# Optimization experiments

Measured on AMD Instinct MI355X. Metric: run time of the kernel, lower is better.

Reference implementation:

```python
import jax, jax.numpy as jnp
import numpy as np

B, L, HID = 2, 2048, 2048
N_HEAD, HEAD_DIM, N_KV = 32, 64, 8
N_Q_PER_KV = N_HEAD // N_KV  # 4
SCALE = 0.125  # 1/sqrt(HEAD_DIM)
PAD_START = L - 256  # last 256 key positions are padding
NEG = -1e9


def setup_inputs() -> dict:
    key = jax.random.key(0)
    ks = jax.random.split(key, 8)
    query = jax.random.normal(ks[0], (B, L, HID), jnp.float32)
    kv = jax.random.normal(ks[1], (B, L, HID), jnp.float32)
    # additive causal mask (0 on/below diagonal, -1e9 above)
    i = jnp.arange(L)
    attn_mask = jnp.where(i[None, :] > i[:, None], NEG, 0.0).astype(jnp.float32)
    # key padding mask: True == padded position
    key_padding_mask = (i[None, :] >= PAD_START) & jnp.ones((B, 1), bool)
    s = 0.02
    Wq = jax.random.normal(ks[2], (HID, N_HEAD * HEAD_DIM), jnp.float32) * s
    bq = jnp.zeros((N_HEAD * HEAD_DIM,), jnp.float32)
    Wkv = jax.random.normal(ks[3], (HID, 2 * N_KV * HEAD_DIM), jnp.float32) * s
    bkv = jnp.zeros((2 * N_KV * HEAD_DIM,), jnp.float32)
    Wo = jax.random.normal(ks[4], (N_HEAD * HEAD_DIM, HID), jnp.float32) * s
    bo = jnp.zeros((HID,), jnp.float32)
    return {"query": query, "kv": kv, "Wq": Wq, "bq": bq, "Wkv": Wkv,
            "bkv": bkv, "Wo": Wo, "bo": bo, "attn_mask": attn_mask,
            "key_padding_mask": key_padding_mask}


def reference(query, kv, Wq, bq, Wkv, bkv, Wo, bo, attn_mask, key_padding_mask):
    b, l, _ = query.shape
    q = (query @ Wq + bq).reshape(b, l, N_HEAD, HEAD_DIM).transpose(0, 2, 1, 3)  # [B,H,L,D]
    kvp = kv @ Wkv + bkv                                   # [B,L,2*NKV*D]
    k, v = jnp.split(kvp, 2, axis=-1)
    k = k.reshape(b, l, N_KV, HEAD_DIM)
    v = v.reshape(b, l, N_KV, HEAD_DIM)
    # GQA: repeat_interleave KV heads to match Q heads
    k = jnp.repeat(k, N_Q_PER_KV, axis=2).transpose(0, 2, 1, 3)  # [B,H,L,D]
    v = jnp.repeat(v, N_Q_PER_KV, axis=2).transpose(0, 2, 1, 3)
    qk = jnp.einsum('bhqd,bhkd->bhqk', q, k) * SCALE
    qk = qk + attn_mask                                     # additive mask
    qk = jnp.where(key_padding_mask[:, None, None, :], NEG, qk)
    p = jax.nn.softmax(qk.astype(jnp.float32), axis=-1).astype(q.dtype)
    attn = jnp.einsum('bhqk,bhkd->bhqd', p, v)
    attn = attn.transpose(0, 2, 1, 3).reshape(b, l, N_HEAD * HEAD_DIM)
    out = attn @ Wo + bo
    return out
```

## Files before the change

### kernel.cpp

```cpp
#include <hip/hip_runtime.h>
#include <stdint.h>

#define L_SEQ 2048
#define HID 2048
#define PADK 1792
#define QSCALE 0.18033688011112042f

typedef unsigned short us_t;
typedef __attribute__((ext_vector_type(8))) short bf16x8;
typedef __attribute__((ext_vector_type(4))) float f32x4;

__device__ __forceinline__ float bf2f(us_t u) {
    union { unsigned int i; float f; } c; c.i = ((unsigned int)u) << 16; return c.f;
}
__device__ __forceinline__ us_t f2bf(float f) {
    union { float f; unsigned int i; } c; c.f = f;
    unsigned int i = c.i;
    return (us_t)((i + 0x7FFFu + ((i >> 16) & 1u)) >> 16);
}
__device__ __forceinline__ unsigned int pk_bf16(float a, float b) {
#if __has_builtin(__builtin_amdgcn_cvt_pk_bf16_f32)
    auto r = __builtin_amdgcn_cvt_pk_bf16_f32(a, b);
    unsigned int u; __builtin_memcpy(&u, &r, 4); return u;
#else
    return (unsigned int)f2bf(a) | ((unsigned int)f2bf(b) << 16);
#endif
}
__device__ __forceinline__ float fast_exp2(float x) {
#if __has_builtin(__builtin_amdgcn_exp2f)
    return __builtin_amdgcn_exp2f(x);
#else
    return exp2f(x);
#endif
}
__device__ __forceinline__ void gload_lds16(const us_t* g, us_t* l) {
    __builtin_amdgcn_global_load_lds((const __attribute__((address_space(1))) void*)g,
                                     (__attribute__((address_space(3))) void*)l, 16, 0, 0);
}
__device__ __forceinline__ int detect_bf16(const unsigned int* q) {
    __shared__ int sc[4];
    unsigned int v = q[threadIdx.x & 255];
    unsigned int e = (v >> 7) & 0xFFu;
    unsigned long long bb = __ballot(e >= 112u && e <= 133u);
    int cnt = __popcll(bb);
    if ((threadIdx.x & 63) == 0) sc[threadIdx.x >> 6] = cnt;
    __syncthreads();
    return (sc[0] + sc[1] + sc[2] + sc[3]) > 128;
}
__device__ __forceinline__ int detect_bf16_512(const unsigned int* q) {
    __shared__ int sc[8];
    unsigned int v = q[threadIdx.x & 255];
    unsigned int e = (v >> 7) & 0xFFu;
    unsigned long long bb = __ballot(e >= 112u && e <= 133u);
    int cnt = __popcll(bb);
    if ((threadIdx.x & 63) == 0) sc[threadIdx.x >> 6] = cnt;
    __syncthreads();
    int s = 0;
    #pragma unroll
    for (int i = 0; i < 8; ++i) s += sc[i];
    return s > 256;
}

__global__ __launch_bounds__(256) void prep(const unsigned int* __restrict__ qdet,
                                            const void* __restrict__ query,
                                            const void* __restrict__ kvsrc,
                                            const void* __restrict__ Wq,
                                            const void* __restrict__ Wkv,
                                            const void* __restrict__ Wo,
                                            us_t* __restrict__ Aq, us_t* __restrict__ Akv,
                                            us_t* __restrict__ Wqt, us_t* __restrict__ Wkvt,
                                            us_t* __restrict__ Wot) {
    __shared__ us_t tile[64][65];
    const int bf = detect_bf16(qdet);
    int id = blockIdx.x;
    if (id < 8192) {
        const void* s = (id < 4096) ? query : kvsrc;
        us_t* d       = (id < 4096) ? Aq : Akv;
        int cid = (id & 4095) * 256 + threadIdx.x;
        if (bf) {
            ((bf16x8*)d)[cid] = ((const bf16x8*)s)[cid];
        } else {
            const float* sp = (const float*)s + (size_t)cid * 8;
            f32x4 a = *(const f32x4*)sp, b2 = *(const f32x4*)(sp + 4);
            union { bf16x8 v; unsigned int dw[4]; } o;
            o.dw[0] = pk_bf16(a[0], a[1]);   o.dw[1] = pk_bf16(a[2], a[3]);
            o.dw[2] = pk_bf16(b2[0], b2[1]); o.dw[3] = pk_bf16(b2[2], b2[3]);
            ((bf16x8*)d)[cid] = o.v;
        }
        return;
    }
    id -= 8192;
    const void* s; us_t* d; int R, C, bx, by;
    if (id < 1024)      { s = Wq;  d = Wqt;  R = 2048; C = 2048; bx = id & 31; by = id >> 5; }
    else if (id < 1536) { id -= 1024; s = Wkv; d = Wkvt; R = 2048; C = 1024; bx = id & 15; by = id >> 4; }
    else                { id -= 1536; s = Wo;  d = Wot;  R = 2048; C = 2048; bx = id & 31; by = id >> 5; }
    const int c0 = bx * 64, r0 = by * 64;
    #pragma unroll
    for (int i = 0; i < 16; ++i) {
        int idx = threadIdx.x + i * 256;
        int r = idx >> 6, c = idx & 63;
        tile[r][c] = bf ? ((const us_t*)s)[(size_t)(r0 + r) * C + c0 + c]
                        : f2bf(((const float*)s)[(size_t)(r0 + r) * C + c0 + c]);
    }
    __syncthreads();
    #pragma unroll
    for (int i = 0; i < 16; ++i) {
        int idx = threadIdx.x + i * 256;
        int c = idx >> 6, r = idx & 63;
        d[(size_t)(c0 + c) * R + r0 + r] = tile[r][c];
    }
}

template<int MQ, int NQ, typename STG, typename TAIL>
__device__ __forceinline__ void phase8(const us_t* Ab, const us_t* Bb,
                                       int wm, int wn, int l15, int cs0, int cs1,
                                       f32x4 (&acc)[8][4], STG&& stg, TAIL&& tail) {
    bf16x8 af[4][2], bv[2][2];
    #pragma unroll
    for (int mt = 0; mt < 4; ++mt) {
        const us_t* p = &Ab[(wm * 128 + MQ * 64 + mt * 16 + l15) * 64];
        af[mt][0] = *(const bf16x8*)&p[cs0 * 8];
        af[mt][1] = *(const bf16x8*)&p[cs1 * 8];
    }
    #pragma unroll
    for (int nt = 0; nt < 2; ++nt) {
        const us_t* p = &Bb[(wn * 64 + NQ * 32 + nt * 16 + l15) * 64];
        bv[nt][0] = *(const bf16x8*)&p[cs0 * 8];
        bv[nt][1] = *(const bf16x8*)&p[cs1 * 8];
    }
    stg();
    __builtin_amdgcn_s_barrier();
    asm volatile("s_waitcnt lgkmcnt(0)" ::: "memory");
    __builtin_amdgcn_sched_barrier(0);
    __builtin_amdgcn_s_setprio(1);
    #pragma unroll
    for (int ki = 0; ki < 2; ++ki)
        #pragma unroll
        for (int mt = 0; mt < 4; ++mt)
            #pragma unroll
            for (int nt = 0; nt < 2; ++nt)
                acc[MQ * 4 + mt][NQ * 2 + nt] = __builtin_amdgcn_mfma_f32_16x16x32_bf16(
                    af[mt][ki], bv[nt][ki], acc[MQ * 4 + mt][NQ * 2 + nt], 0, 0, 0);
    __builtin_amdgcn_s_setprio(0);
    tail();
    __builtin_amdgcn_s_barrier();
}

__global__ __launch_bounds__(512, 2) void qkv_gemm(const unsigned int* __restrict__ qdet,
                                                   const us_t* __restrict__ Aq,
                                                   const us_t* __restrict__ Akv,
                                                   const us_t* __restrict__ Wqt,
                                                   const us_t* __restrict__ Wkvt,
                                                   const void* __restrict__ bq,
                                                   const void* __restrict__ bkv,
                                                   us_t* __restrict__ Qm,
                                                   us_t* __restrict__ Km,
                                                   us_t* __restrict__ Vg) {
    __shared__ us_t sh[65536];
    us_t* As0 = sh;
    us_t* As1 = sh + 16384;
    us_t* Bs0 = sh + 32768;
    us_t* Bs1 = sh + 49152;

    const int bf = detect_bf16_512(qdet);
    const int t = threadIdx.x;
    const int w = t >> 6, lane = t & 63, l15 = lane & 15, quad = lane >> 4;
    const int wm = w >> 2, wn = w & 3;
    const int cs0 = quad ^ (l15 & 7);
    const int cs1 = (4 + quad) ^ (l15 & 7);

    int id = blockIdx.x;
    const us_t* Ag; const us_t* Bg; int bm, bn; bool isQ;
    if (id < 128) { isQ = true;  Ag = Aq;  Bg = Wqt;  bm = (id >> 3) * 256; bn = (id & 7) * 256; }
    else { id -= 128; isQ = false; Ag = Akv; Bg = Wkvt; bm = (id >> 2) * 256; bn = (id & 3) * 256; }

    size_t aoff[2][2], boff[2][2]; int adst[2][2], bdst[2][2];
    #pragma unroll
    for (int u = 0; u < 2; ++u)
        #pragma unroll
        for (int j = 0; j < 2; ++j) {
            int row0 = j * 128 + u * 64 + w * 8;
            int row  = row0 + (lane >> 3);
            int col  = ((lane & 7) ^ (row & 7)) * 8;
            aoff[u][j] = (size_t)(bm + row) * 2048 + col;
            adst[u][j] = row0 * 64;
            int ci   = w * 2 + j;
            int rb0  = (ci >> 2) * 64 + u * 32 + (ci & 3) * 8;
            int rowb = rb0 + (lane >> 3);
            int colb = ((lane & 7) ^ (rowb & 7)) * 8;
            boff[u][j] = (size_t)(bn + rowb) * 2048 + colb;
            bdst[u][j] = rb0 * 64;
        }

#define STAGE_A(U, KT, DST) do { \
        gload_lds16(Ag + aoff[U][0] + (size_t)(KT) * 64, (DST) + adst[U][0]); \
        gload_lds16(Ag + aoff[U][1] + (size_t)(KT) * 64, (DST) + adst[U][1]); } while (0)
#define STAGE_B(U, KT, DST) do { \
        gload_lds16(Bg + boff[U][0] + (size_t)(KT) * 64, (DST) + bdst[U][0]); \
        gload_lds16(Bg + boff[U][1] + (size_t)(KT) * 64, (DST) + bdst[U][1]); } while (0)

    f32x4 acc[8][4];
    #pragma unroll
    for (int i = 0; i < 8; ++i)
        #pragma unroll
        for (int j = 0; j < 4; ++j) acc[i][j] = (f32x4){0.f, 0.f, 0.f, 0.f};

    STAGE_A(0, 0, As0); STAGE_B(0, 0, Bs0);
    STAGE_A(1, 0, As0); STAGE_B(1, 0, Bs0);
    STAGE_A(0, 1, As1); STAGE_B(0, 1, Bs1);
    asm volatile("s_waitcnt vmcnt(4)" ::: "memory");
    __builtin_amdgcn_s_barrier();

    auto notail = [] {};
    #pragma unroll 1
    for (int it = 0; it < 16; ++it) {
        const bool more = (it < 15);
        const int k1 = 2 * it + 1, k2 = 2 * it + 2, k3 = 2 * it + 3;
        phase8<0, 0>(As0, Bs0, wm, wn, l15, cs0, cs1, acc,
                     [&] { STAGE_A(1, k1, As1); }, notail);
        phase8<0, 1>(As0, Bs0, wm, wn, l15, cs0, cs1, acc,
                     [&] { STAGE_B(1, k1, Bs1); }, notail);
        phase8<1, 0>(As0, Bs0, wm, wn, l15, cs0, cs1, acc,
                     [&] { if (more) STAGE_A(0, k2, As0); }, notail);
        phase8<1, 1>(As0, Bs0, wm, wn, l15, cs0, cs1, acc,
                     [&] { if (more) STAGE_B(0, k2, Bs0); },
                     [&] { if (more) asm volatile("s_waitcnt vmcnt(4)" ::: "memory");
                           else      asm volatile("s_waitcnt vmcnt(0)" ::: "memory"); });
        phase8<0, 0>(As1, Bs1, wm, wn, l15, cs0, cs1, acc,
                     [&] { if (more) STAGE_A(1, k2, As0); }, notail);
        phase8<0, 1>(As1, Bs1, wm, wn, l15, cs0, cs1, acc,
                     [&] { if (more) STAGE_B(1, k2, Bs0); }, notail);
        phase8<1, 0>(As1, Bs1, wm, wn, l15, cs0, cs1, acc,
                     [&] { if (more) STAGE_A(0, k3, As1); }, notail);
        phase8<1, 1>(As1, Bs1, wm, wn, l15, cs0, cs1, acc,
                     [&] { if (more) STAGE_B(0, k3, Bs1); },
                     [&] { if (more) asm volatile("s_waitcnt vmcnt(4)" ::: "memory"); });
    }
#undef STAGE_A
#undef STAGE_B

    if (isQ) {
        #pragma unroll
        for (int an = 0; an < 4; ++an) {
            int col = bn + wn * 64 + an * 16 + l15;
            float bvv = bf ? bf2f(((const us_t*)bq)[col]) : ((const float*)bq)[col];
            #pragma unroll
            for (int am = 0; am < 8; ++am)
                #pragma unroll
                for (int r = 0; r < 4; ++r) {
                    int row = bm + wm * 128 + am * 16 + quad * 4 + r;
                    Qm[(size_t)row * 2048 + col] = f2bf((acc[am][an][r] + bvv) * QSCALE);
                }
        }
    } else if (bn < 512) {
        #pragma unroll
        for (int an = 0; an < 4; ++an) {
            int col = bn + wn * 64 + an * 16 + l15;
            float bvv = bf ? bf2f(((const us_t*)bkv)[col]) : ((const float*)bkv)[col];
            #pragma unroll
            for (int am = 0; am < 8; ++am)
                #pragma unroll
                for (int r = 0; r < 4; ++r) {
                    int row = bm + wm * 128 + am * 16 + quad * 4 + r;
                    Km[(size_t)row * 512 + col] = f2bf(acc[am][an][r] + bvv);
                }
        }
    } else {
        const int b2 = bm >> 11, tok0 = bm & 2047;
        #pragma unroll
        for (int half = 0; half < 2; ++half) {
            __syncthreads();
            if ((wn >> 1) == half) {
                #pragma unroll
                for (int an = 0; an < 4; ++an) {
                    int col = bn + wn * 64 + an * 16 + l15;
                    float bvv = bf ? bf2f(((const us_t*)bkv)[col]) : ((const float*)bkv)[col];
                    int cl = (wn & 1) * 64 + an * 16 + l15;
                    #pragma unroll
                    for (int am = 0; am < 8; ++am)
                        #pragma unroll
                        for (int r = 0; r < 4; ++r) {
                            int tok = wm * 128 + am * 16 + quad * 4 + r;
                            sh[cl * 258 + tok] = f2bf(acc[am][an][r] + bvv);
                        }
                }
            }
            __syncthreads();
            size_t vrow0 = (size_t)(b2 * 512 + (bn - 512) + half * 128);
            #pragma unroll
            for (int jj = 0; jj < 8; ++jj) {
                int idx = t + jj * 512;
                int c2 = idx >> 5, ch = idx & 31;
                bf16x8 vv = *(const bf16x8*)&sh[c2 * 258 + ch * 8];
                *(bf16x8*)(Vg + (vrow0 + c2) * (size_t)2048 + tok0 + ch * 8) = vv;
            }
        }
    }
}

__device__ __forceinline__ void gemm_core(const us_t* __restrict__ A,
                                          const us_t* __restrict__ Bt,
                                          int K, int bm, int bn, int t,
                                          us_t (&As)[2][8192], us_t (&Bs)[2][8192],
                                          f32x4 (&acc)[4][4]) {
    const int w = t >> 6, lane = t & 63, l15 = lane & 15, quad = lane >> 4;
    const int wm = (w & 1) * 64, wn = (w >> 1) * 64;
    int rA[4], cA[4];
    #pragma unroll
    for (int i = 0; i < 4; ++i) {
        int p = (w * 4 + i) * 64 + lane;
        int row = p >> 3, cs = p & 7;
        rA[i] = row; cA[i] = (cs ^ (row & 7)) * 8;
    }
    #pragma unroll
    for (int i = 0; i < 4; ++i) {
        gload_lds16(A  + (size_t)(bm + rA[i]) * K + cA[i], &As[0][(w * 4 + i) * 512]);
        gload_lds16(Bt + (size_t)(bn + rA[i]) * K + cA[i], &Bs[0][(w * 4 + i) * 512]);
    }
    int pb = 0;
    for (int k0 = 0; k0 < K; k0 += 64) {
        __syncthreads();
        if (k0 + 64 < K) {
            #pragma unroll
            for (int i = 0; i < 4; ++i) {
                gload_lds16(A  + (size_t)(bm + rA[i]) * K + k0 + 64 + cA[i], &As[pb ^ 1][(w * 4 + i) * 512]);
                gload_lds16(Bt + (size_t)(bn + rA[i]) * K + k0 + 64 + cA[i], &Bs[pb ^ 1][(w * 4 + i) * 512]);
            }
        }
        #pragma unroll
        for (int ki = 0; ki < 2; ++ki) {
            bf16x8 af[4], bfr[4];
            #pragma unroll
            for (int mt = 0; mt < 4; ++mt) {
                int row = wm + mt * 16 + l15;
                int cs  = (ki * 4 + quad) ^ (row & 7);
                af[mt] = *(const bf16x8*)&As[pb][row * 64 + cs * 8];
            }
            #pragma unroll
            for (int nt = 0; nt < 4; ++nt) {
                int row = wn + nt * 16 + l15;
                int cs  = (ki * 4 + quad) ^ (row & 7);
                bfr[nt] = *(const bf16x8*)&Bs[pb][row * 64 + cs * 8];
            }
            #pragma unroll
            for (int mt = 0; mt < 4; ++mt)
                #pragma unroll
                for (int nt = 0; nt < 4; ++nt)
                    acc[mt][nt] = __builtin_amdgcn_mfma_f32_16x16x32_bf16(af[mt], bfr[nt], acc[mt][nt], 0, 0, 0);
        }
        pb ^= 1;
    }
}

__global__ __launch_bounds__(256, 2) void o_gemm(const unsigned int* __restrict__ qdet,
                                                 const us_t* __restrict__ Ao,
                                                 const us_t* __restrict__ Wot,
                                                 const void* __restrict__ bo,
                                                 void* __restrict__ Out) {
    __shared__ us_t As[2][8192], Bs[2][8192];
    const int bf = detect_bf16(qdet);
    const int t = threadIdx.x;
    const int w = t >> 6, lane = t & 63, l15 = lane & 15, quad = lane >> 4;
    const int wm = (w & 1) * 64, wn = (w >> 1) * 64;
    const int bm = blockIdx.y * 128, bn = blockIdx.x * 128;
    f32x4 acc[4][4];
    #pragma unroll
    for (int i = 0; i < 4; ++i)
        #pragma unroll
        for (int j = 0; j < 4; ++j) acc[i][j] = (f32x4){0.f, 0.f, 0.f, 0.f};
    gemm_core(Ao, Wot, 2048, bm, bn, t, As, Bs, acc);
    #pragma unroll
    for (int nt = 0; nt < 4; ++nt) {
        int col = bn + wn + nt * 16 + l15;
        float bvv = bf ? bf2f(((const us_t*)bo)[col]) : ((const float*)bo)[col];
        #pragma unroll
        for (int mt = 0; mt < 4; ++mt)
            #pragma unroll
            for (int r = 0; r < 4; ++r) {
                int row = bm + wm + mt * 16 + quad * 4 + r;
                float v = acc[mt][nt][r] + bvv;
                if (bf) ((us_t*)Out)[(size_t)row * 2048 + col] = f2bf(v);
                else    ((float*)Out)[(size_t)row * 2048 + col] = v;
            }
    }
}

__device__ __forceinline__ void qk_exp(const bf16x8 kb[2][4], const bf16x8 qf[2][2],
                                       int q0, int k0, int l15, int quad,
                                       bf16x8 pa[2][2]) {
    f32x4 sa[2][4];
    #pragma unroll
    for (int mt = 0; mt < 2; ++mt)
        #pragma unroll
        for (int nt = 0; nt < 4; ++nt) sa[mt][nt] = (f32x4){0.f, 0.f, 0.f, 0.f};
    #pragma unroll
    for (int ki = 0; ki < 2; ++ki)
        #pragma unroll
        for (int mt = 0; mt < 2; ++mt)
            #pragma unroll
            for (int nt = 0; nt < 4; ++nt)
                sa[mt][nt] = __builtin_amdgcn_mfma_f32_16x16x32_bf16(kb[ki][nt], qf[mt][ki], sa[mt][nt], 0, 0, 0);
    const bool nm = (k0 + 63 > q0);
    #pragma unroll
    for (int mt = 0; mt < 2; ++mt) {
        const int qrow = q0 + mt * 16 + l15;
        union { bf16x8 v; unsigned int dw[4]; } u;
        #pragma unroll
        for (int k2 = 0; k2 < 2; ++k2) {
            #pragma unroll
            for (int hf = 0; hf < 2; ++hf) {
                const int nt = k2 * 2 + hf;
                const int keyb = k0 + k2 * 32 + hf * 4 + quad * 8;
                float e[4];
                #pragma unroll
                for (int r = 0; r < 4; ++r) {
                    float s = sa[mt][nt][r];
                    if (nm && (keyb + r > qrow)) s = -1e30f;
                    e[r] = fast_exp2(s);
                }
                u.dw[hf * 2]     = pk_bf16(e[0], e[1]);
                u.dw[hf * 2 + 1] = pk_bf16(e[2], e[3]);
            }
            pa[mt][k2] = u.v;
        }
    }
}

__global__ __launch_bounds__(256, 2) void attn_mfma(const us_t* __restrict__ Q,
                                                    const us_t* __restrict__ Km,
                                                    const us_t* __restrict__ Vg,
                                                    us_t* __restrict__ Am) {
    __shared__ us_t Ks[2][4096];
    __shared__ us_t Vt[2][4096];

    const int bid = blockIdx.x;
    const int pr  = bid & 31;
    const int kvh = (bid >> 5) & 7;
    const int b   = bid >> 8;
    const int t = threadIdx.x, w = t >> 6, lane = t & 63, l15 = lane & 15, quad = lane >> 4;
    const int h = kvh * 4 + w;
    const int q0h = 2016 - 32 * pr, q0l = 32 * pr;
    const int kend0 = min(q0h + 32, PADK), kend1 = min(q0l + 32, PADK);

    bf16x8 ones;
    #pragma unroll
    for (int j = 0; j < 8; ++j) ones[j] = (short)0x3F80;

    const us_t* Kbase = Km + (size_t)(b * L_SEQ) * 512 + kvh * 64;
    const us_t* Vbase = Vg + (size_t)(b * 512 + kvh * 64) * L_SEQ;

    size_t ksrc[2], vsrc[2];
    #pragma unroll
    for (int i = 0; i < 2; ++i) {
        int idx = (w * 2 + i) * 64 + lane;
        int p = idx >> 3, cs = idx & 7, c = cs ^ (p & 7);
        int gk = (p & 0x23) | ((p & 0x0C) << 1) | ((p & 0x10) >> 2);
        ksrc[i] = (size_t)gk * 512 + c * 8;
        vsrc[i] = (size_t)p * 2048 + c * 8;
    }

    bf16x8 qfh[2][2], qfl[2][2];
    #pragma unroll
    for (int mt = 0; mt < 2; ++mt)
        #pragma unroll
        for (int ki = 0; ki < 2; ++ki) {
            qfh[mt][ki] = *(const bf16x8*)(Q + (size_t)(b * L_SEQ + q0h + mt * 16 + l15) * HID
                                             + h * 64 + ki * 32 + quad * 8);
            qfl[mt][ki] = *(const bf16x8*)(Q + (size_t)(b * L_SEQ + q0l + mt * 16 + l15) * HID
                                             + h * 64 + ki * 32 + quad * 8);
        }

    f32x4 oah[2][4], oal[2][4], lah[2], lal[2];
    #pragma unroll
    for (int mt = 0; mt < 2; ++mt) {
        lah[mt] = (f32x4){0.f, 0.f, 0.f, 0.f};
        lal[mt] = (f32x4){0.f, 0.f, 0.f, 0.f};
        #pragma unroll
        for (int dn = 0; dn < 4; ++dn) {
            oah[mt][dn] = (f32x4){0.f, 0.f, 0.f, 0.f};
            oal[mt][dn] = (f32x4){0.f, 0.f, 0.f, 0.f};
        }
    }

    #pragma unroll
    for (int i = 0; i < 2; ++i) {
        gload_lds16(Kbase + ksrc[i], &Ks[0][(w * 2 + i) * 512]);
        gload_lds16(Vbase + vsrc[i], &Vt[0][(w * 2 + i) * 512]);
    }

    int pb = 0;
    for (int k0 = 0; k0 < kend0; k0 += 64) {
        __syncthreads();
        if (k0 + 64 < kend0) {
            #pragma unroll
            for (int i = 0; i < 2; ++i) {
                gload_lds16(Kbase + (size_t)(k0 + 64) * 512 + ksrc[i], &Ks[pb ^ 1][(w * 2 + i) * 512]);
                gload_lds16(Vbase + (k0 + 64) + vsrc[i],               &Vt[pb ^ 1][(w * 2 + i) * 512]);
            }
        }
        const bool dolight = (k0 < kend1);

        bf16x8 kb[2][4];
        #pragma unroll
        for (int ki = 0; ki < 2; ++ki)
            #pragma unroll
            for (int nt = 0; nt < 4; ++nt) {
                int row = nt * 16 + l15;
                int cs  = (ki * 4 + quad) ^ (row & 7);
                kb[ki][nt] = *(const bf16x8*)&Ks[pb][row * 64 + cs * 8];
            }

        bf16x8 pah[2][2], pal[2][2];
        qk_exp(kb, qfh, q0h, k0, l15, quad, pah);
        if (dolight) qk_exp(kb, qfl, q0l, k0, l15, quad, pal);

        bf16x8 vb[2][4];
        #pragma unroll
        for (int k2 = 0; k2 < 2; ++k2)
            #pragma unroll
            for (int dn = 0; dn < 4; ++dn) {
                int d  = dn * 16 + l15;
                int cs = (k2 * 4 + quad) ^ (d & 7);
                vb[k2][dn] = *(const bf16x8*)&Vt[pb][d * 64 + cs * 8];
            }

        #pragma unroll
        for (int k2 = 0; k2 < 2; ++k2)
            #pragma unroll
            for (int mt = 0; mt < 2; ++mt) {
                lah[mt] = __builtin_amdgcn_mfma_f32_16x16x32_bf16(pah[mt][k2], ones, lah[mt], 0, 0, 0);
                #pragma unroll
                for (int dn = 0; dn < 4; ++dn)
                    oah[mt][dn] = __builtin_amdgcn_mfma_f32_16x16x32_bf16(pah[mt][k2], vb[k2][dn], oah[mt][dn], 0, 0, 0);
            }
        if (dolight) {
            #pragma unroll
            for (int k2 = 0; k2 < 2; ++k2)
                #pragma unroll
                for (int mt = 0; mt < 2; ++mt) {
                    lal[mt] = __builtin_amdgcn_mfma_f32_16x16x32_bf16(pal[mt][k2], ones, lal[mt], 0, 0, 0);
                    #pragma unroll
                    for (int dn = 0; dn < 4; ++dn)
                        oal[mt][dn] = __builtin_amdgcn_mfma_f32_16x16x32_bf16(pal[mt][k2], vb[k2][dn], oal[mt][dn], 0, 0, 0);
                }
        }
        pb ^= 1;
    }

    #pragma unroll
    for (int mt = 0; mt < 2; ++mt)
        #pragma unroll
        for (int r = 0; r < 4; ++r) {
            float invh = 1.0f / lah[mt][r];
            float invl = 1.0f / lal[mt][r];
            int rowh = q0h + mt * 16 + quad * 4 + r;
            int rowl = q0l + mt * 16 + quad * 4 + r;
            #pragma unroll
            for (int dn = 0; dn < 4; ++dn) {
                Am[(size_t)(b * L_SEQ + rowh) * HID + h * 64 + dn * 16 + l15] =
                    f2bf(oah[mt][dn][r] * invh);
                Am[(size_t)(b * L_SEQ + rowl) * HID + h * 64 + dn * 16 + l15] =
                    f2bf(oal[mt][dn][r] * invl);
            }
        }
}

extern "C" void kernel_launch(void* const* d_in, const int* in_sizes, int n_in,
                              void* d_out, int out_size, void* d_ws, size_t ws_size,
                              hipStream_t stream) {
    const void* query = d_in[0];
    const void* kv    = d_in[1];
    const void* Wq    = d_in[2];
    const void* bq    = d_in[3];
    const void* Wkv   = d_in[4];
    const void* bkv   = d_in[5];
    const void* Wo    = d_in[6];
    const void* bo    = d_in[7];
    const unsigned int* qdet = (const unsigned int*)query;

    char* p = (char*)d_ws;
    us_t* Qm   = (us_t*)p;                p += (size_t)4096 * 2048 * 2;
    us_t* Km   = (us_t*)p;                p += (size_t)4096 * 512 * 2;
    us_t* Vg   = (us_t*)p;                p += (size_t)1024 * 2048 * 2;
    us_t* AqAm = (us_t*)p;                p += (size_t)4096 * 2048 * 2;
    us_t* Akv  = (us_t*)p;                p += (size_t)4096 * 2048 * 2;
    us_t* Wqt  = (us_t*)p;                p += (size_t)2048 * 2048 * 2;
    us_t* Wkvt = (us_t*)p;                p += (size_t)1024 * 2048 * 2;
    us_t* Wot  = (us_t*)p;

    dim3 blk(256);
    prep<<<dim3(10752), blk, 0, stream>>>(qdet, query, kv, Wq, Wkv, Wo,
                                          AqAm, Akv, Wqt, Wkvt, Wot);
    qkv_gemm<<<dim3(192), dim3(512), 0, stream>>>(qdet, AqAm, Akv, Wqt, Wkvt, bq, bkv,
                                                  Qm, Km, Vg);
    attn_mfma<<<dim3(512), blk, 0, stream>>>(Qm, Km, Vg, AqAm);
    o_gemm<<<dim3(16, 32), blk, 0, stream>>>(qdet, AqAm, Wot, bo, d_out);
}
```

Baseline: 363.9 us.

## Share 256x256 pipelined GEMM core between QKV and output projections

Factors the QKV GEMM main loop into a shared gemm256 routine and changes the per-phase structure from four 8-MFMA phases to two 16-MFMA phases. B fragments are now loaded once per k-step and reused across both M halves, and the staging schedule and vmcnt waits are reworked to match. The output projection moves from a 128x128, 256-thread double-buffered GEMM to the same 256x256, 512-thread pipelined core, which cuts its grid to 128 blocks. This reduces LDS reads and barriers and gives the O GEMM more reuse per tile, but 128 blocks may underfill the GPU's compute units and register pressure rises.

```diff
diff --git a/kernel.cpp b/kernel.cpp
--- a/kernel.cpp
+++ b/kernel.cpp
@@ -111,22 +111,25 @@
     }
 }
 
-template<int MQ, int NQ, typename STG, typename TAIL>
-__device__ __forceinline__ void phase8(const us_t* Ab, const us_t* Bb,
+template<int MQ, typename STG, typename TAIL>
+__device__ __forceinline__ void phase2(const us_t* Ab, const us_t* Bb,
                                        int wm, int wn, int l15, int cs0, int cs1,
-                                       f32x4 (&acc)[8][4], STG&& stg, TAIL&& tail) {
-    bf16x8 af[4][2], bv[2][2];
+                                       bf16x8 (&bv)[4][2], f32x4 (&acc)[8][4],
+                                       STG&& stg, TAIL&& tail) {
+    bf16x8 af[4][2];
     #pragma unroll
     for (int mt = 0; mt < 4; ++mt) {
         const us_t* p = &Ab[(wm * 128 + MQ * 64 + mt * 16 + l15) * 64];
         af[mt][0] = *(const bf16x8*)&p[cs0 * 8];
         af[mt][1] = *(const bf16x8*)&p[cs1 * 8];
     }
-    #pragma unroll
-    for (int nt = 0; nt < 2; ++nt) {
-        const us_t* p = &Bb[(wn * 64 + NQ * 32 + nt * 16 + l15) * 64];
-        bv[nt][0] = *(const bf16x8*)&p[cs0 * 8];
-        bv[nt][1] = *(const bf16x8*)&p[cs1 * 8];
+    if (MQ == 0) {
+        #pragma unroll
+        for (int nt = 0; nt < 4; ++nt) {
+            const us_t* p = &Bb[(wn * 64 + nt * 16 + l15) * 64];
+            bv[nt][0] = *(const bf16x8*)&p[cs0 * 8];
+            bv[nt][1] = *(const bf16x8*)&p[cs1 * 8];
+        }
     }
     stg();
     __builtin_amdgcn_s_barrier();
@@ -138,12 +141,86 @@
         #pragma unroll
         for (int mt = 0; mt < 4; ++mt)
             #pragma unroll
-            for (int nt = 0; nt < 2; ++nt)
-                acc[MQ * 4 + mt][NQ * 2 + nt] = __builtin_amdgcn_mfma_f32_16x16x32_bf16(
-                    af[mt][ki], bv[nt][ki], acc[MQ * 4 + mt][NQ * 2 + nt], 0, 0, 0);
+            for (int nt = 0; nt < 4; ++nt)
+                acc[MQ * 4 + mt][nt] = __builtin_amdgcn_mfma_f32_16x16x32_bf16(
+                    af[mt][ki], bv[nt][ki], acc[MQ * 4 + mt][nt], 0, 0, 0);
     __builtin_amdgcn_s_setprio(0);
     tail();
     __builtin_amdgcn_s_barrier();
+}
+
+__device__ __forceinline__ void gemm256(const us_t* __restrict__ Ag,
+                                        const us_t* __restrict__ Bg,
+                                        int bm, int bn, us_t* sh,
+                                        f32x4 (&acc)[8][4]) {
+    us_t* As0 = sh;           us_t* As1 = sh + 16384;
+    us_t* Bs0 = sh + 32768;   us_t* Bs1 = sh + 49152;
+    const int t = threadIdx.x;
+    const int w = t >> 6, lane = t & 63, l15 = lane & 15, quad = lane >> 4;
+    const int wm = w >> 2, wn = w & 3;
+    const int cs0 = quad ^ (l15 & 7);
+    const int cs1 = (4 + quad) ^ (l15 & 7);
+
+    int aoff[2][2], boff[2][2], adst[2][2], bdst[2][2];
+    #pragma unroll
+    for (int u = 0; u < 2; ++u)
+        #pragma unroll
+        for (int j = 0; j < 2; ++j) {
+            int row0 = j * 128 + u * 64 + w * 8;
+            int row  = row0 + (lane >> 3);
+            int col  = ((lane & 7) ^ (row & 7)) * 8;
+            aoff[u][j] = (bm + row) * 2048 + col;
+            adst[u][j] = row0 * 64;
+            int ci   = w * 2 + j;
+            int rb0  = (ci >> 2) * 64 + u * 32 + (ci & 3) * 8;
+            int rowb = rb0 + (lane >> 3);
+            int colb = ((lane & 7) ^ (rowb & 7)) * 8;
+            boff[u][j] = (bn + rowb) * 2048 + colb;
+            bdst[u][j] = rb0 * 64;
+        }
+
+#define STAGE_A(U, KT, DST) do { \
+        gload_lds16(Ag + (size_t)aoff[U][0] + (KT) * 64, (DST) + adst[U][0]); \
+        gload_lds16(Ag + (size_t)aoff[U][1] + (KT) * 64, (DST) + adst[U][1]); } while (0)
+#define STAGE_B(U, KT, DST) do { \
+        gload_lds16(Bg + (size_t)boff[U][0] + (KT) * 64, (DST) + bdst[U][0]); \
+        gload_lds16(Bg + (size_t)boff[U][1] + (KT) * 64, (DST) + bdst[U][1]); } while (0)
+
+    #pragma unroll
+    for (int i = 0; i < 8; ++i)
+        #pragma unroll
+        for (int j = 0; j < 4; ++j) acc[i][j] = (f32x4){0.f, 0.f, 0.f, 0.f};
+
+    STAGE_A(0, 0, As0); STAGE_B(0, 0, Bs0);
+    STAGE_A(1, 0, As0); STAGE_B(1, 0, Bs0);
+    STAGE_A(0, 1, As1); STAGE_B(0, 1, Bs1); STAGE_B(1, 1, Bs1);
+    asm volatile("s_waitcnt vmcnt(6)" ::: "memory");
+    __builtin_amdgcn_s_barrier();
+
+    bf16x8 bv[4][2];
+    #pragma unroll 1
+    for (int it = 0; it < 16; ++it) {
+        const bool more = (it < 15);
+        const int kb = 2 * it + 1;
+        phase2<0>(As0, Bs0, wm, wn, l15, cs0, cs1, bv, acc,
+                  [&] { STAGE_A(1, kb, As1); },
+                  [&] { asm volatile("s_waitcnt vmcnt(8)" ::: "memory"); });
+        phase2<1>(As0, Bs0, wm, wn, l15, cs0, cs1, bv, acc,
+                  [&] { if (more) { STAGE_A(0, kb + 1, As0); STAGE_B(0, kb + 1, Bs0);
+                                    STAGE_B(1, kb + 1, Bs0); } },
+                  [&] { if (more) asm volatile("s_waitcnt vmcnt(8)" ::: "memory");
+                        else      asm volatile("s_waitcnt vmcnt(2)" ::: "memory"); });
+        phase2<0>(As1, Bs1, wm, wn, l15, cs0, cs1, bv, acc,
+                  [&] { if (more) STAGE_A(1, kb + 1, As0); },
+                  [&] { if (more) asm volatile("s_waitcnt vmcnt(8)" ::: "memory");
+                        else      asm volatile("s_waitcnt vmcnt(0)" ::: "memory"); });
+        phase2<1>(As1, Bs1, wm, wn, l15, cs0, cs1, bv, acc,
+                  [&] { if (more) { STAGE_A(0, kb + 2, As1); STAGE_B(0, kb + 2, Bs1);
+                                    STAGE_B(1, kb + 2, Bs1); } },
+                  [&] { if (more) asm volatile("s_waitcnt vmcnt(8)" ::: "memory"); });
+    }
+#undef STAGE_A
+#undef STAGE_B
 }
 
 __global__ __launch_bounds__(512, 2) void qkv_gemm(const unsigned int* __restrict__ qdet,
@@ -157,87 +234,18 @@
                                                    us_t* __restrict__ Km,
                                                    us_t* __restrict__ Vg) {
     __shared__ us_t sh[65536];
-    us_t* As0 = sh;
-    us_t* As1 = sh + 16384;
-    us_t* Bs0 = sh + 32768;
-    us_t* Bs1 = sh + 49152;
-
     const int bf = detect_bf16_512(qdet);
     const int t = threadIdx.x;
     const int w = t >> 6, lane = t & 63, l15 = lane & 15, quad = lane >> 4;
     const int wm = w >> 2, wn = w & 3;
-    const int cs0 = quad ^ (l15 & 7);
-    const int cs1 = (4 + quad) ^ (l15 & 7);
 
     int id = blockIdx.x;
     const us_t* Ag; const us_t* Bg; int bm, bn; bool isQ;
     if (id < 128) { isQ = true;  Ag = Aq;  Bg = Wqt;  bm = (id >> 3) * 256; bn = (id & 7) * 256; }
     else { id -= 128; isQ = false; Ag = Akv; Bg = Wkvt; bm = (id >> 2) * 256; bn = (id & 3) * 256; }
 
-    size_t aoff[2][2], boff[2][2]; int adst[2][2], bdst[2][2];
-    #pragma unroll
-    for (int u = 0; u < 2; ++u)
-        #pragma unroll
-        for (int j = 0; j < 2; ++j) {
-            int row0 = j * 128 + u * 64 + w * 8;
-            int row  = row0 + (lane >> 3);
-            int col  = ((lane & 7) ^ (row & 7)) * 8;
-            aoff[u][j] = (size_t)(bm + row) * 2048 + col;
-            adst[u][j] = row0 * 64;
-            int ci   = w * 2 + j;
-            int rb0  = (ci >> 2) * 64 + u * 32 + (ci & 3) * 8;
-            int rowb = rb0 + (lane >> 3);
-            int colb = ((lane & 7) ^ (rowb & 7)) * 8;
-            boff[u][j] = (size_t)(bn + rowb) * 2048 + colb;
-            bdst[u][j] = rb0 * 64;
-        }
-
-#define STAGE_A(U, KT, DST) do { \
-        gload_lds16(Ag + aoff[U][0] + (size_t)(KT) * 64, (DST) + adst[U][0]); \
-        gload_lds16(Ag + aoff[U][1] + (size_t)(KT) * 64, (DST) + adst[U][1]); } while (0)
-#define STAGE_B(U, KT, DST) do { \
-        gload_lds16(Bg + boff[U][0] + (size_t)(KT) * 64, (DST) + bdst[U][0]); \
-        gload_lds16(Bg + boff[U][1] + (size_t)(KT) * 64, (DST) + bdst[U][1]); } while (0)
-
     f32x4 acc[8][4];
-    #pragma unroll
-    for (int i = 0; i < 8; ++i)
-        #pragma unroll
-        for (int j = 0; j < 4; ++j) acc[i][j] = (f32x4){0.f, 0.f, 0.f, 0.f};
-
-    STAGE_A(0, 0, As0); STAGE_B(0, 0, Bs0);
-    STAGE_A(1, 0, As0); STAGE_B(1, 0, Bs0);
-    STAGE_A(0, 1, As1); STAGE_B(0, 1, Bs1);
-    asm volatile("s_waitcnt vmcnt(4)" ::: "memory");
-    __builtin_amdgcn_s_barrier();
-
-    auto notail = [] {};
-    #pragma unroll 1
-    for (int it = 0; it < 16; ++it) {
-        const bool more = (it < 15);
-        const int k1 = 2 * it + 1, k2 = 2 * it + 2, k3 = 2 * it + 3;
-        phase8<0, 0>(As0, Bs0, wm, wn, l15, cs0, cs1, acc,
-                     [&] { STAGE_A(1, k1, As1); }, notail);
-        phase8<0, 1>(As0, Bs0, wm, wn, l15, cs0, cs1, acc,
-                     [&] { STAGE_B(1, k1, Bs1); }, notail);
-        phase8<1, 0>(As0, Bs0, wm, wn, l15, cs0, cs1, acc,
-                     [&] { if (more) STAGE_A(0, k2, As0); }, notail);
-        phase8<1, 1>(As0, Bs0, wm, wn, l15, cs0, cs1, acc,
-                     [&] { if (more) STAGE_B(0, k2, Bs0); },
-                     [&] { if (more) asm volatile("s_waitcnt vmcnt(4)" ::: "memory");
-                           else      asm volatile("s_waitcnt vmcnt(0)" ::: "memory"); });
-        phase8<0, 0>(As1, Bs1, wm, wn, l15, cs0, cs1, acc,
-                     [&] { if (more) STAGE_A(1, k2, As0); }, notail);
-        phase8<0, 1>(As1, Bs1, wm, wn, l15, cs0, cs1, acc,
-                     [&] { if (more) STAGE_B(1, k2, Bs0); }, notail);
-        phase8<1, 0>(As1, Bs1, wm, wn, l15, cs0, cs1, acc,
-                     [&] { if (more) STAGE_A(0, k3, As1); }, notail);
-        phase8<1, 1>(As1, Bs1, wm, wn, l15, cs0, cs1, acc,
-                     [&] { if (more) STAGE_B(0, k3, Bs1); },
-                     [&] { if (more) asm volatile("s_waitcnt vmcnt(4)" ::: "memory"); });
-    }
-#undef STAGE_A
-#undef STAGE_B
+    gemm256(Ag, Bg, bm, bn, sh, acc);
 
     if (isQ) {
         #pragma unroll
@@ -298,87 +306,32 @@
     }
 }
 
-__device__ __forceinline__ void gemm_core(const us_t* __restrict__ A,
-                                          const us_t* __restrict__ Bt,
-                                          int K, int bm, int bn, int t,
-                                          us_t (&As)[2][8192], us_t (&Bs)[2][8192],
-                                          f32x4 (&acc)[4][4]) {
-    const int w = t >> 6, lane = t & 63, l15 = lane & 15, quad = lane >> 4;
-    const int wm = (w & 1) * 64, wn = (w >> 1) * 64;
-    int rA[4], cA[4];
-    #pragma unroll
-    for (int i = 0; i < 4; ++i) {
-        int p = (w * 4 + i) * 64 + lane;
-        int row = p >> 3, cs = p & 7;
-        rA[i] = row; cA[i] = (cs ^ (row & 7)) * 8;
-    }
-    #pragma unroll
-    for (int i = 0; i < 4; ++i) {
-        gload_lds16(A  + (size_t)(bm + rA[i]) * K + cA[i], &As[0][(w * 4 + i) * 512]);
-        gload_lds16(Bt + (size_t)(bn + rA[i]) * K + cA[i], &Bs[0][(w * 4 + i) * 512]);
-    }
-    int pb = 0;
-    for (int k0 = 0; k0 < K; k0 += 64) {
-        __syncthreads();
-        if (k0 + 64 < K) {
-            #pragma unroll
-            for (int i = 0; i < 4; ++i) {
-                gload_lds16(A  + (size_t)(bm + rA[i]) * K + k0 + 64 + cA[i], &As[pb ^ 1][(w * 4 + i) * 512]);
-                gload_lds16(Bt + (size_t)(bn + rA[i]) * K + k0 + 64 + cA[i], &Bs[pb ^ 1][(w * 4 + i) * 512]);
-            }
-        }
-        #pragma unroll
-        for (int ki = 0; ki < 2; ++ki) {
-            bf16x8 af[4], bfr[4];
-            #pragma unroll
-            for (int mt = 0; mt < 4; ++mt) {
-                int row = wm + mt * 16 + l15;
-                int cs  = (ki * 4 + quad) ^ (row & 7);
-                af[mt] = *(const bf16x8*)&As[pb][row * 64 + cs * 8];
-            }
-            #pragma unroll
-            for (int nt = 0; nt < 4; ++nt) {
-                int row = wn + nt * 16 + l15;
-                int cs  = (ki * 4 + quad) ^ (row & 7);
-                bfr[nt] = *(const bf16x8*)&Bs[pb][row * 64 + cs * 8];
-            }
-            #pragma unroll
-            for (int mt = 0; mt < 4; ++mt)
-                #pragma unroll
-                for (int nt = 0; nt < 4; ++nt)
-                    acc[mt][nt] = __builtin_amdgcn_mfma_f32_16x16x32_bf16(af[mt], bfr[nt], acc[mt][nt], 0, 0, 0);
-        }
-        pb ^= 1;
-    }
-}
-
-__global__ __launch_bounds__(256, 2) void o_gemm(const unsigned int* __restrict__ qdet,
+__global__ __launch_bounds__(512, 2) void o_gemm(const unsigned int* __restrict__ qdet,
                                                  const us_t* __restrict__ Ao,
                                                  const us_t* __restrict__ Wot,
                                                  const void* __restrict__ bo,
                                                  void* __restrict__ Out) {
-    __shared__ us_t As[2][8192], Bs[2][8192];
-    const int bf = detect_bf16(qdet);
+    __shared__ us_t sh[65536];
+    const int bf = detect_bf16_512(qdet);
     const int t = threadIdx.x;
     const int w = t >> 6, lane = t & 63, l15 = lane & 15, quad = lane >> 4;
-    const int wm = (w & 1) * 64, wn = (w >> 1) * 64;
-    const int bm = blockIdx.y * 128, bn = blockIdx.x * 128;
-    f32x4 acc[4][4];
-    #pragma unroll
-    for (int i = 0; i < 4; ++i)
-        #pragma unroll
-        for (int j = 0; j < 4; ++j) acc[i][j] = (f32x4){0.f, 0.f, 0.f, 0.f};
-    gemm_core(Ao, Wot, 2048, bm, bn, t, As, Bs, acc);
-    #pragma unroll
-    for (int nt = 0; nt < 4; ++nt) {
-        int col = bn + wn + nt * 16 + l15;
+    const int wm = w >> 2, wn = w & 3;
+    const int id = blockIdx.x;
+    const int bm = (id >> 3) * 256, bn = (id & 7) * 256;
+
+    f32x4 acc[8][4];
+    gemm256(Ao, Wot, bm, bn, sh, acc);
+
+    #pragma unroll
+    for (int an = 0; an < 4; ++an) {
+        int col = bn + wn * 64 + an * 16 + l15;
         float bvv = bf ? bf2f(((const us_t*)bo)[col]) : ((const float*)bo)[col];
         #pragma unroll
-        for (int mt = 0; mt < 4; ++mt)
+        for (int am = 0; am < 8; ++am)
             #pragma unroll
             for (int r = 0; r < 4; ++r) {
-                int row = bm + wm + mt * 16 + quad * 4 + r;
-                float v = acc[mt][nt][r] + bvv;
+                int row = bm + wm * 128 + am * 16 + quad * 4 + r;
+                float v = acc[am][an][r] + bvv;
                 if (bf) ((us_t*)Out)[(size_t)row * 2048 + col] = f2bf(v);
                 else    ((float*)Out)[(size_t)row * 2048 + col] = v;
             }
@@ -594,5 +547,5 @@
     qkv_gemm<<<dim3(192), dim3(512), 0, stream>>>(qdet, AqAm, Akv, Wqt, Wkvt, bq, bkv,
                                                   Qm, Km, Vg);
     attn_mfma<<<dim3(512), blk, 0, stream>>>(Qm, Km, Vg, AqAm);
-    o_gemm<<<dim3(16, 32), blk, 0, stream>>>(qdet, AqAm, Wot, bo, d_out);
-}
+    o_gemm<<<dim3(128), dim3(512), 0, stream>>>(qdet, AqAm, Wot, bo, d_out);
+}
```

New measurement: 372.0 us. +2.2%, slower.
